# Performance work log

Measured on AMD Instinct MI355X. Metric: run time of the kernel, lower is better.

## Reference

```python
import jax, jax.numpy as jnp
import numpy as np

D, W, B, T = 128, 512, 512, 512

# Tsit5 Butcher tableau (Tsitouras 2011), as used by diffrax.Tsit5
A21 = 0.161
A31, A32 = -0.008480655492356989, 0.335480655492357
A41, A42, A43 = 2.8971530571054935, -6.359448489975075, 4.3622954328695815
A51, A52, A53, A54 = 5.325864828439257, -11.748883564062828, 7.4955393428898365, -0.09249506636175525
A61, A62, A63, A64, A65 = 5.86145544294642, -12.92096931784711, 8.159367898576159, -0.071584973281401, -0.028269050394068383
B1, B2, B3, B4, B5, B6 = 0.09646076681806523, 0.01, 0.4798896504144996, 1.379008574103742, -3.290069515436081, 2.324710524099774


def setup_inputs() -> dict:
    key = jax.random.key(0)
    ks = jax.random.split(key, 8)
    u = lambda k, shape, s: jax.random.uniform(k, shape, minval=-s, maxval=s, dtype=jnp.float32)
    s3 = float(np.sqrt(1.0 / 3.0))
    sD = float(1.0 / np.sqrt(D))
    sW = float(1.0 / np.sqrt(W))
    return {
        "ts": jnp.arange(T, dtype=jnp.float32) * 1e-3,  # uniform save grid, dt0 = 1e-3
        "yi": jax.random.normal(ks[0], (B, 1, D), dtype=jnp.float32),
        "w1": u(ks[1], (W, D), sD), "b1": u(ks[2], (W,), sD),
        "w2": u(ks[3], (W, W), sW), "b2": u(ks[4], (W,), sW),
        "w3": u(ks[5], (D, W), sW), "b3": u(ks[6], (D,), sW),
        "A": u(ks[7], (D, D), s3),
    }


def reference(ts, yi, w1, b1, w2, b2, w3, b3, A):
    # StabilizedFunc: f(y) = MLP(y) + A @ y, batched over B
    def vf(y):  # y: [B, D]
        h = jnp.tanh(y @ w1.T + b1)
        h = jnp.tanh(h @ w2.T + b2)
        return h @ w3.T + b3 + y @ A.T

    def step(y, h):  # one constant-step Tsit5 step of size h
        k1 = vf(y)
        k2 = vf(y + h * (A21 * k1))
        k3 = vf(y + h * (A31 * k1 + A32 * k2))
        k4 = vf(y + h * (A41 * k1 + A42 * k2 + A43 * k3))
        k5 = vf(y + h * (A51 * k1 + A52 * k2 + A53 * k3 + A54 * k4))
        k6 = vf(y + h * (A61 * k1 + A62 * k2 + A63 * k3 + A64 * k4 + A65 * k5))
        y_new = y + h * (B1 * k1 + B2 * k2 + B3 * k3 + B4 * k4 + B5 * k5 + B6 * k6)
        return y_new, y_new

    y0 = yi[:, 0, :]                      # [B, D]
    dts = ts[1:] - ts[:-1]                # [T-1]
    _, ys = jax.lax.scan(step, y0, dts)   # ys: [T-1, B, D]
    out = jnp.concatenate([y0[None], ys], axis=0)  # [T, B, D]
    return jnp.transpose(out, (1, 0, 2))  # [B, T, D]
```

## Files before the change

### kernel.cpp

```cpp
#include <hip/hip_runtime.h>
#include <stdint.h>


#define Dd 128
#define Ww 512
#define Tt 512
#define NSTEP 511
#define NWG 32
#define NTHR 512

#define GRP_USH 1024
#define WAVE_USH (50 * GRP_USH)
#define WS_TOT (8 * WAVE_USH)

#define H1F 0
#define H2F 16384
#define Y0F 32768
#define Y1F 36864
#define ATF 40960
#define DTF 41152
#define SMEMB 43200

typedef __attribute__((ext_vector_type(8))) __bf16 bf16x8;
typedef __attribute__((ext_vector_type(4))) float f32x4;

__device__ __forceinline__ unsigned short f2b(float f) {
  union { float f; unsigned int u; } v; v.f = f;
  return (unsigned short)((v.u + 0x7fffu + ((v.u >> 16) & 1u)) >> 16);
}
__device__ __forceinline__ float fast_tanh(float x) {
  x = fminf(fmaxf(x, -15.f), 15.f);
  float e = __expf(2.f * x);
  return (e - 1.f) / (e + 1.f);
}
__device__ __forceinline__ int fragaddr(int m, int n) {
  return ((n >> 5) << 10) + ((((n >> 3) & 3) * 16 + m) << 4) + ((n & 7) << 1);
}

__device__ const float RKC[48] = {
  0.161f, 0.f, 0.f, 0.f, 0.f, 0.f, 0.f, 0.f,
  -0.008480655492356989f, 0.335480655492357f, 0.f, 0.f, 0.f, 0.f, 0.f, 0.f,
  2.8971530571054935f, -6.359448489975075f, 4.3622954328695815f, 0.f, 0.f, 0.f, 0.f, 0.f,
  5.325864828439257f, -11.748883564062828f, 7.4955393428898365f,
  -0.09249506636175525f, 0.f, 0.f, 0.f, 0.f,
  5.86145544294642f, -12.92096931784711f, 8.159367898576159f,
  -0.071584973281401f, -0.028269050394068383f, 0.f, 0.f, 0.f,
  0.09646076681806523f, 0.01f, 0.4798896504144996f, 1.379008574103742f,
  -3.290069515436081f, 2.324710524099774f, 0.f, 0.f
};

#define LDG1(dst, off_) \
  asm volatile("global_load_dwordx4 %0, %1, off" \
               : "=&v"(dst) : "v"(gsb + (off_)))

#define ISSUE_ITER(bi, mm) do { \
    LDG1(bb[bi][0], (((mm) % 25) * 4096)); \
    LDG1(bb[bi][1], (((mm) % 25) * 4096 + 1024)); \
    LDG1(bb[bi][2], (((mm) % 25) * 4096 + 2048)); \
    LDG1(bb[bi][3], (((mm) % 25) * 4096 + 3072)); } while (0)

#define VMW12() do { asm volatile("s_waitcnt vmcnt(12)" ::: "memory"); \
                     __builtin_amdgcn_sched_barrier(0); } while (0)
#define LBAR() do { asm volatile("s_waitcnt lgkmcnt(0)" ::: "memory"); \
                    __builtin_amdgcn_s_barrier(); } while (0)

#define MFMA(a, b, c) __builtin_amdgcn_mfma_f32_16x16x32_bf16((a), (b), (c), 0, 0, 0)
#define CPK(kd) do { kd[0]=kk[0]; kd[1]=kk[1]; kd[2]=kk[2]; kd[3]=kk[3]; } while (0)

__global__ void prep_kernel(const float* __restrict__ w1,
                            const float* __restrict__ w2,
                            const float* __restrict__ w3,
                            const float* __restrict__ Am,
                            unsigned short* __restrict__ wsb) {
  for (int i = blockIdx.x * blockDim.x + threadIdx.x; i < WS_TOT;
       i += gridDim.x * blockDim.x) {
    const int j    = i & 7;
    const int L    = (i >> 3) & 63;
    const int l16  = L & 15;
    const int q    = L >> 4;
    const int tile = (i >> 9) & 1;
    const int g    = (i >> 10) % 50;
    const int w    = i / WAVE_USH;
    float v;
    if (g < 8) {
      const int nt = (g & 1) * 2 + tile, ks = g >> 1;
      v = w1[(w * 64 + nt * 16 + l16) * Dd + ks * 32 + q * 8 + j];
    } else if (g < 40) {
      const int gg = g - 8;
      const int nt = (gg & 1) * 2 + tile, ks = gg >> 1;
      v = w2[(w * 64 + nt * 16 + l16) * Ww + ks * 32 + q * 8 + j];
    } else if (g < 48) {
      const int kcol = 2 * (g - 40) + tile;
      v = w3[(w * 16 + l16) * Ww + kcol * 32 + q * 8 + j];
    } else {
      const int kcol = 2 * (g - 48) + tile;
      v = Am[(w * 16 + l16) * Dd + kcol * 32 + q * 8 + j];
    }
    wsb[i] = f2b(v);
  }
}

__global__ void __launch_bounds__(NTHR, 1)
ode_kernel(const float* __restrict__ ts,
           const float* __restrict__ yi,
           const float* __restrict__ b1,
           const float* __restrict__ b2,
           const float* __restrict__ b3,
           float* __restrict__ out,
           const unsigned short* __restrict__ wsb)
{
  extern __shared__ char smem_c[];

  const int tid  = threadIdx.x;
  const int wid  = tid >> 6;
  const int lane = tid & 63;
  const int l16  = lane & 15;
  const int quad = lane >> 4;
  const int lob  = lane << 4;
  const int b0   = blockIdx.x * 16;

  char* h1f = smem_c + H1F;
  char* h2f = smem_c + H2F;

  const char* gsb = (const char*)(wsb + wid * WAVE_USH) + lob;

  if (tid < 48) *(float*)(smem_c + ATF + (tid << 2)) = RKC[tid];
  for (int i = tid; i < NSTEP; i += NTHR)
    *(float*)(smem_c + DTF + (i << 2)) = ts[i + 1] - ts[i];

  float b1v[4], b2v[4];
  #pragma unroll
  for (int nt = 0; nt < 4; ++nt) {
    b1v[nt] = b1[(wid << 6) + (nt << 4) + l16];
    b2v[nt] = b2[(wid << 6) + (nt << 4) + l16];
  }
  const float b3v = b3[(wid << 4) + l16];

  int hwaddr[4];
  #pragma unroll
  for (int nt = 0; nt < 4; ++nt)
    hwaddr[nt] = fragaddr(quad << 2, (wid << 6) + (nt << 4) + l16);
  const int nC = (wid << 4) + l16;
  const int ydst = fragaddr(quad << 2, nC);

  float y[4];
  #pragma unroll
  for (int r = 0; r < 4; ++r) {
    y[r] = yi[(size_t)(b0 + (quad << 2) + r) * Dd + nC];
    *(unsigned short*)(smem_c + Y0F + ydst + (r << 4)) = f2b(y[r]);
    out[(size_t)(b0 + (quad << 2) + r) * (Tt * Dd) + nC] = y[r];
  }

  float k0[4] = {0,0,0,0}, k1[4] = {0,0,0,0}, k2[4] = {0,0,0,0},
        k3[4] = {0,0,0,0}, k4[4] = {0,0,0,0}, k5[4] = {0,0,0,0};

  __syncthreads();

  bf16x8 bb[5][4];
  ISSUE_ITER(0, 0); ISSUE_ITER(1, 1); ISSUE_ITER(2, 2); ISSUE_ITER(3, 3);

  #pragma unroll 1
  for (int t = 0; t < NSTEP; ++t) {
    const float hdt = *(const float*)(smem_c + DTF + (t << 2));

    #pragma unroll 1
    for (int s = 0; s < 6; ++s) {
      const char* ybr = smem_c + ((s & 1) ? Y1F : Y0F);
      char*       ybw = smem_c + ((s & 1) ? Y0F : Y1F);

      LBAR();

      {
        f32x4 accA[4];
        #pragma unroll
        for (int nt = 0; nt < 4; ++nt) { f32x4 z = {0.f,0.f,0.f,0.f}; accA[nt] = z; }
        #pragma unroll
        for (int m = 0; m < 4; ++m) {
          VMW12();
          bf16x8 af = *(const bf16x8*)(ybr + (m << 10) + lob);
          ISSUE_ITER((m + 4) % 5, m + 4);
          #pragma unroll
          for (int nt = 0; nt < 4; ++nt)
            accA[nt] = MFMA(af, bb[m][nt], accA[nt]);
        }
        #pragma unroll
        for (int nt = 0; nt < 4; ++nt)
          #pragma unroll
          for (int r = 0; r < 4; ++r)
            *(unsigned short*)(h1f + hwaddr[nt] + (r << 4)) =
                f2b(fast_tanh(accA[nt][r] + b1v[nt]));
      }
      LBAR();

      {
        f32x4 accB[4];
        #pragma unroll
        for (int nt = 0; nt < 4; ++nt) { f32x4 z = {0.f,0.f,0.f,0.f}; accB[nt] = z; }
        #pragma unroll
        for (int ks = 0; ks < 16; ++ks) {
          VMW12();
          bf16x8 af = *(const bf16x8*)(h1f + (ks << 10) + lob);
          ISSUE_ITER((ks + 8) % 5, ks + 8);
          #pragma unroll
          for (int nt = 0; nt < 4; ++nt)
            accB[nt] = MFMA(af, bb[(ks + 4) % 5][nt], accB[nt]);
        }
        #pragma unroll
        for (int nt = 0; nt < 4; ++nt)
          #pragma unroll
          for (int r = 0; r < 4; ++r)
            *(unsigned short*)(h2f + hwaddr[nt] + (r << 4)) =
                f2b(fast_tanh(accB[nt][r] + b2v[nt]));
      }
      LBAR();

      {
        f32x4 accC0 = {0.f, 0.f, 0.f, 0.f};
        f32x4 accC1 = {0.f, 0.f, 0.f, 0.f};
        #pragma unroll
        for (int cc = 0; cc < 5; ++cc) {
          VMW12();
          bf16x8 a0, a1, a2, a3;
          if (cc < 4) {
            a0 = *(const bf16x8*)(h2f + ((4*cc + 0) << 10) + lob);
            a1 = *(const bf16x8*)(h2f + ((4*cc + 1) << 10) + lob);
            a2 = *(const bf16x8*)(h2f + ((4*cc + 2) << 10) + lob);
            a3 = *(const bf16x8*)(h2f + ((4*cc + 3) << 10) + lob);
          } else {
            a0 = *(const bf16x8*)(ybr + (0 << 10) + lob);
            a1 = *(const bf16x8*)(ybr + (1 << 10) + lob);
            a2 = *(const bf16x8*)(ybr + (2 << 10) + lob);
            a3 = *(const bf16x8*)(ybr + (3 << 10) + lob);
          }
          ISSUE_ITER((cc + 24) % 5, cc + 24);
          accC0 = MFMA(a0, bb[cc][0], accC0);
          accC1 = MFMA(a1, bb[cc][1], accC1);
          accC0 = MFMA(a2, bb[cc][2], accC0);
          accC1 = MFMA(a3, bb[cc][3], accC1);
        }
        float kk[4];
        #pragma unroll
        for (int r = 0; r < 4; ++r) kk[r] = accC0[r] + accC1[r] + b3v;
        switch (s) {
          case 0: CPK(k0); break;
          case 1: CPK(k1); break;
          case 2: CPK(k2); break;
          case 3: CPK(k3); break;
          case 4: CPK(k4); break;
          default: CPK(k5); break;
        }
      }

      {
        const float* cp = (const float*)(smem_c + ATF + (s << 5));
        const float c0 = cp[0], c1 = cp[1], c2 = cp[2];
        const float c3 = cp[3], c4 = cp[4], c5 = cp[5];
        float a_[4];
        #pragma unroll
        for (int r = 0; r < 4; ++r)
          a_[r] = y[r] + hdt * (c0*k0[r] + c1*k1[r] + c2*k2[r] +
                                c3*k3[r] + c4*k4[r] + c5*k5[r]);
        #pragma unroll
        for (int r = 0; r < 4; ++r)
          *(unsigned short*)(ybw + ydst + (r << 4)) = f2b(a_[r]);
        if (s == 5) {
          #pragma unroll
          for (int r = 0; r < 4; ++r) {
            y[r] = a_[r];
            out[(size_t)(b0 + (quad << 2) + r) * (Tt * Dd) +
                (size_t)(t + 1) * Dd + nC] = a_[r];
          }
        }
      }
    }
  }

  asm volatile("s_waitcnt vmcnt(0) lgkmcnt(0)" ::: "memory");
}

extern "C" void kernel_launch(void* const* d_in, const int* in_sizes, int n_in,
                              void* d_out, int out_size, void* d_ws, size_t ws_size,
                              hipStream_t stream) {
  (void)in_sizes; (void)n_in; (void)out_size; (void)ws_size;

  const float* ts = (const float*)d_in[0];
  const float* yi = (const float*)d_in[1];
  const float* w1 = (const float*)d_in[2];
  const float* b1 = (const float*)d_in[3];
  const float* w2 = (const float*)d_in[4];
  const float* b2 = (const float*)d_in[5];
  const float* w3 = (const float*)d_in[6];
  const float* b3 = (const float*)d_in[7];
  const float* Am = (const float*)d_in[8];
  float* outp = (float*)d_out;
  unsigned short* wsb = (unsigned short*)d_ws;

  (void)hipFuncSetAttribute(reinterpret_cast<const void*>(ode_kernel),
                            hipFuncAttributeMaxDynamicSharedMemorySize,
                            SMEMB);

  prep_kernel<<<400, 256, 0, stream>>>(w1, w2, w3, Am, wsb);
  ode_kernel<<<dim3(NWG), dim3(NTHR), SMEMB, stream>>>(
      ts, yi, b1, b2, b3, outp, wsb);
}
```

Before: 42.52 ms.

## Stream half of weight fragments through per-wave LDS ring via global_load_lds

Half of each weight fragment group is now loaded straight from global memory into a per-wave LDS ring buffer with global_load_lds, and the other half still goes to registers. The register prefetch buffer shrinks, the prefetch depth drops from 4 to 3 iterations, and the vmcnt wait threshold changes to match. The goal is to relieve register pressure while keeping the weight stream overlapped with MFMA work. In exchange it adds LDS reads and an lgkmcnt(0) wait on every iteration, and raises LDS use to about 125KB.

Result: faster. 35.20 ms (-17.2%).

```diff
diff --git a/kernel.cpp b/kernel.cpp
--- a/kernel.cpp
+++ b/kernel.cpp
@@ -13,13 +13,14 @@
 #define WAVE_USH (50 * GRP_USH)
 #define WS_TOT (8 * WAVE_USH)
 
-#define H1F 0
-#define H2F 16384
-#define Y0F 32768
-#define Y1F 36864
-#define ATF 40960
-#define DTF 41152
-#define SMEMB 43200
+#define RING_PER_WAVE 10240
+#define H1F 81920
+#define H2F 98304
+#define Y0F 114688
+#define Y1F 118784
+#define ATF 122880
+#define DTF 123072
+#define SMEMB 125120
 
 typedef __attribute__((ext_vector_type(8))) __bf16 bf16x8;
 typedef __attribute__((ext_vector_type(4))) float f32x4;
@@ -49,17 +50,25 @@
   -3.290069515436081f, 2.324710524099774f, 0.f, 0.f
 };
 
+#define GLDS(gp, lp) __builtin_amdgcn_global_load_lds( \
+    (const __attribute__((address_space(1))) unsigned int*)(const void*)(gp), \
+    (__attribute__((address_space(3))) unsigned int*)(void*)(lp), 16, 0, 0)
+
 #define LDG1(dst, off_) \
   asm volatile("global_load_dwordx4 %0, %1, off" \
-               : "=&v"(dst) : "v"(gsb + (off_)))
-
-#define ISSUE_ITER(bi, mm) do { \
-    LDG1(bb[bi][0], (((mm) % 25) * 4096)); \
-    LDG1(bb[bi][1], (((mm) % 25) * 4096 + 1024)); \
-    LDG1(bb[bi][2], (((mm) % 25) * 4096 + 2048)); \
-    LDG1(bb[bi][3], (((mm) % 25) * 4096 + 3072)); } while (0)
-
-#define VMW12() do { asm volatile("s_waitcnt vmcnt(12)" ::: "memory"); \
+               : "=&v"(dst) : "v"(gsbb + (off_)))
+
+#define ITS(mm) (((mm) % 25) * 4096)
+#define BI(mm) ((mm) % 5)
+#define ISS(mm) do { \
+    GLDS(gsbb + ITS(mm),        ring_w + BI(mm) * 2048); \
+    GLDS(gsbb + ITS(mm) + 1024, ring_w + BI(mm) * 2048 + 1024); \
+    LDG1(bbd[BI(mm)][0], ITS(mm) + 2048); \
+    LDG1(bbd[BI(mm)][1], ITS(mm) + 3072); } while (0)
+
+#define VMW8() do { asm volatile("s_waitcnt vmcnt(8)" ::: "memory"); \
+                    __builtin_amdgcn_sched_barrier(0); } while (0)
+#define LGKM0() do { asm volatile("s_waitcnt lgkmcnt(0)" ::: "memory"); \
                      __builtin_amdgcn_sched_barrier(0); } while (0)
 #define LBAR() do { asm volatile("s_waitcnt lgkmcnt(0)" ::: "memory"); \
                     __builtin_amdgcn_s_barrier(); } while (0)
@@ -119,10 +128,11 @@
   const int lob  = lane << 4;
   const int b0   = blockIdx.x * 16;
 
+  char* ring_w = smem_c + wid * RING_PER_WAVE;
   char* h1f = smem_c + H1F;
   char* h2f = smem_c + H2F;
 
-  const char* gsb = (const char*)(wsb + wid * WAVE_USH) + lob;
+  const char* gsbb = (const char*)(wsb + wid * WAVE_USH) + lob;
 
   if (tid < 48) *(float*)(smem_c + ATF + (tid << 2)) = RKC[tid];
   for (int i = tid; i < NSTEP; i += NTHR)
@@ -156,8 +166,8 @@
 
   __syncthreads();
 
-  bf16x8 bb[5][4];
-  ISSUE_ITER(0, 0); ISSUE_ITER(1, 1); ISSUE_ITER(2, 2); ISSUE_ITER(3, 3);
+  bf16x8 bbd[5][2];
+  ISS(0); ISS(1); ISS(2);
 
   #pragma unroll 1
   for (int t = 0; t < NSTEP; ++t) {
@@ -176,12 +186,16 @@
         for (int nt = 0; nt < 4; ++nt) { f32x4 z = {0.f,0.f,0.f,0.f}; accA[nt] = z; }
         #pragma unroll
         for (int m = 0; m < 4; ++m) {
-          VMW12();
-          bf16x8 af = *(const bf16x8*)(ybr + (m << 10) + lob);
-          ISSUE_ITER((m + 4) % 5, m + 4);
-          #pragma unroll
-          for (int nt = 0; nt < 4; ++nt)
-            accA[nt] = MFMA(af, bb[m][nt], accA[nt]);
+          VMW8();
+          bf16x8 af  = *(const bf16x8*)(ybr + (m << 10) + lob);
+          bf16x8 bv0 = *(const bf16x8*)(ring_w + BI(m) * 2048 + lob);
+          bf16x8 bv1 = *(const bf16x8*)(ring_w + BI(m) * 2048 + 1024 + lob);
+          LGKM0();
+          ISS(m + 3);
+          accA[0] = MFMA(af, bv0, accA[0]);
+          accA[1] = MFMA(af, bv1, accA[1]);
+          accA[2] = MFMA(af, bbd[BI(m)][0], accA[2]);
+          accA[3] = MFMA(af, bbd[BI(m)][1], accA[3]);
         }
         #pragma unroll
         for (int nt = 0; nt < 4; ++nt)
@@ -198,12 +212,17 @@
         for (int nt = 0; nt < 4; ++nt) { f32x4 z = {0.f,0.f,0.f,0.f}; accB[nt] = z; }
         #pragma unroll
         for (int ks = 0; ks < 16; ++ks) {
-          VMW12();
-          bf16x8 af = *(const bf16x8*)(h1f + (ks << 10) + lob);
-          ISSUE_ITER((ks + 8) % 5, ks + 8);
-          #pragma unroll
-          for (int nt = 0; nt < 4; ++nt)
-            accB[nt] = MFMA(af, bb[(ks + 4) % 5][nt], accB[nt]);
+          const int m = 4 + ks;
+          VMW8();
+          bf16x8 af  = *(const bf16x8*)(h1f + (ks << 10) + lob);
+          bf16x8 bv0 = *(const bf16x8*)(ring_w + BI(m) * 2048 + lob);
+          bf16x8 bv1 = *(const bf16x8*)(ring_w + BI(m) * 2048 + 1024 + lob);
+          LGKM0();
+          ISS(m + 3);
+          accB[0] = MFMA(af, bv0, accB[0]);
+          accB[1] = MFMA(af, bv1, accB[1]);
+          accB[2] = MFMA(af, bbd[BI(m)][0], accB[2]);
+          accB[3] = MFMA(af, bbd[BI(m)][1], accB[3]);
         }
         #pragma unroll
         for (int nt = 0; nt < 4; ++nt)
@@ -219,7 +238,8 @@
         f32x4 accC1 = {0.f, 0.f, 0.f, 0.f};
         #pragma unroll
         for (int cc = 0; cc < 5; ++cc) {
-          VMW12();
+          const int m = 20 + cc;
+          VMW8();
           bf16x8 a0, a1, a2, a3;
           if (cc < 4) {
             a0 = *(const bf16x8*)(h2f + ((4*cc + 0) << 10) + lob);
@@ -232,11 +252,14 @@
             a2 = *(const bf16x8*)(ybr + (2 << 10) + lob);
             a3 = *(const bf16x8*)(ybr + (3 << 10) + lob);
           }
-          ISSUE_ITER((cc + 24) % 5, cc + 24);
-          accC0 = MFMA(a0, bb[cc][0], accC0);
-          accC1 = MFMA(a1, bb[cc][1], accC1);
-          accC0 = MFMA(a2, bb[cc][2], accC0);
-          accC1 = MFMA(a3, bb[cc][3], accC1);
+          bf16x8 bv0 = *(const bf16x8*)(ring_w + BI(m) * 2048 + lob);
+          bf16x8 bv1 = *(const bf16x8*)(ring_w + BI(m) * 2048 + 1024 + lob);
+          LGKM0();
+          ISS(m + 3);
+          accC0 = MFMA(a0, bv0, accC0);
+          accC1 = MFMA(a1, bv1, accC1);
+          accC0 = MFMA(a2, bbd[BI(m)][0], accC0);
+          accC1 = MFMA(a3, bbd[BI(m)][1], accC1);
         }
         float kk[4];
         #pragma unroll
```
